# Performance work log

Measured on AMD Instinct MI355X. Metric: run time of the kernel, lower is better.

The kernel has to match this reference:

```python
import jax, jax.numpy as jnp
import numpy as np

B, T, K, H = 4, 2048, 128, 8
MASK = True


def setup_inputs() -> dict:
    key = jax.random.key(0)
    ks = jax.random.split(key, 6)
    s = 0.02
    return {
        "x": jax.random.normal(ks[0], (B, T, K), dtype=jnp.float32),
        "Wq": jax.random.normal(ks[1], (K, H * K), dtype=jnp.float32) * s,
        "Wk": jax.random.normal(ks[2], (K, H * K), dtype=jnp.float32) * s,
        "Wv": jax.random.normal(ks[3], (K, H * K), dtype=jnp.float32) * s,
        "Wu": jax.random.normal(ks[4], (H * K, K), dtype=jnp.float32) * s,
        "bu": jnp.zeros((K,), dtype=jnp.float32),
    }


def reference(x, Wq, Wk, Wv, Wu, bu):
    b, t, k = x.shape
    h = H
    q = (x @ Wq).reshape(b, t, h, k)
    kk = (x @ Wk).reshape(b, t, h, k)
    # module pre-scales values by k**-0.25 (idiosyncratic but faithful)
    v = (x @ Wv).reshape(b, t, h, k) * (k ** -0.25)
    # scores [b, h, t, t], scaled by k**-0.5
    scores = jnp.einsum('bthd,bshd->bhts', q, kk) * (k ** -0.5)
    if MASK:
        causal = jnp.tril(jnp.ones((t, t), dtype=bool))
        scores = jnp.where(causal, scores, -jnp.inf)
    w = jax.nn.softmax(scores, axis=-1)
    out = jnp.einsum('bhts,bshd->bthd', w, v).reshape(b, t, h * k)
    return out @ Wu + bu
```

## Files before the change

### kernel.cpp

```cpp
#include <hip/hip_runtime.h>
#include <hip/hip_bf16.h>
#include <math.h>

#define B_ 4
#define T_ 2048
#define D_ 128
#define H_ 8
#define BT_ 8192
#define HD_ 1024

typedef __attribute__((ext_vector_type(8))) short bf16x8;
typedef __attribute__((ext_vector_type(4))) float f32x4;

__device__ __forceinline__ short f2bf(float f) {
  union { float f; unsigned u; } v; v.f = f;
  return (short)((v.u + 0x8000u) >> 16);
}

#if __has_builtin(__builtin_amdgcn_exp2f)
#define EXP2F(x) __builtin_amdgcn_exp2f(x)
#else
#define EXP2F(x) exp2f(x)
#endif

#define QSCALE 0.12752040242046492f
#define VSCALE 0.29730177875068026f

__device__ __forceinline__ void gld16(const short* g, short* l) {
  __builtin_amdgcn_global_load_lds(
      (const __attribute__((address_space(1))) void*)g,
      (__attribute__((address_space(3))) void*)l, 16, 0, 0);
}

__global__ __launch_bounds__(256) void prep(
    const float* __restrict__ x, const float* __restrict__ Wq,
    const float* __restrict__ Wk, const float* __restrict__ Wv,
    short* __restrict__ xbf, short* __restrict__ WT)
{
  __shared__ __align__(16) short Tt[128*128];
  const int tid = threadIdx.x;
  const int id = blockIdx.x;
  if (id < 24) {
    const int wsel = id >> 3, nt = id & 7;
    const float* W = (wsel == 0) ? Wq : (wsel == 1) ? Wk : Wv;
    #pragma unroll 4
    for (int i = tid; i < 4096; i += 256) {
      int k = i >> 5, n4 = (i & 31) << 2;
      float4 v = *(const float4*)&W[(size_t)k * HD_ + nt*128 + n4];
      float vv[4] = {v.x, v.y, v.z, v.w};
      #pragma unroll
      for (int j = 0; j < 4; j++) {
        int n = n4 + j;
        Tt[n*128 + (((k >> 3) ^ (n & 15)) << 3) + (k & 7)] = f2bf(vv[j]);
      }
    }
    __syncthreads();
    short* dst = WT + (size_t)id * 16384;
    #pragma unroll 2
    for (int i = tid; i < 2048; i += 256)
      *(bf16x8*)&dst[i*8] = *(bf16x8*)&Tt[i*8];
  } else {
    const int xb = id - 24;
    const float* xs = x + (size_t)xb * 16384;
    short* dst = xbf + (size_t)xb * 16384;
    #pragma unroll 4
    for (int i = tid; i < 4096; i += 256) {
      float4 v = ((const float4*)xs)[i];
      int row = i >> 5, c = (i & 31) >> 1, half = i & 1;
      short4 p;
      p.x = f2bf(v.x); p.y = f2bf(v.y); p.z = f2bf(v.z); p.w = f2bf(v.w);
      *(short4*)&dst[(row*16 + (c ^ (row & 15)))*8 + half*4] = p;
    }
  }
}

__global__ __launch_bounds__(256, 2) void qkv_proj(
    const short* __restrict__ xbf, const short* __restrict__ WT,
    short* __restrict__ Qw, short* __restrict__ Kw, short* __restrict__ Vw)
{
  __shared__ __align__(16) short As[16384];
  __shared__ __align__(16) short Bs[16384];
  const int tid = threadIdx.x;
  const int w = tid >> 6, lane = tid & 63, quad = lane >> 4, l16 = lane & 15;
  const int m0 = blockIdx.x * 128;

  {
    const short* asrc = xbf + (size_t)blockIdx.x * 16384;
    const short* bsrc = WT + (size_t)blockIdx.y * 16384;
    const int so = w*4096 + lane*8;
    #pragma unroll
    for (int cc = 0; cc < 8; cc++) {
      gld16(asrc + so + cc*512, &As[w*4096 + cc*512]);
      gld16(bsrc + so + cc*512, &Bs[w*4096 + cc*512]);
    }
  }
  __syncthreads();

  const int wm = (w & 1) * 64, wn = (w >> 1) * 64;
  f32x4 acc[4][4];
  #pragma unroll
  for (int a = 0; a < 4; a++)
    #pragma unroll
    for (int b = 0; b < 4; b++) acc[a][b] = (f32x4){0.f, 0.f, 0.f, 0.f};

  #pragma unroll
  for (int kk = 0; kk < 4; kk++) {
    const int swz = ((kk*4 + quad) ^ l16) << 3;
    bf16x8 af[4], bfv[4];
    #pragma unroll
    for (int mi = 0; mi < 4; mi++) af[mi]  = *(bf16x8*)&As[(wm + mi*16 + l16)*128 + swz];
    #pragma unroll
    for (int ni = 0; ni < 4; ni++) bfv[ni] = *(bf16x8*)&Bs[(wn + ni*16 + l16)*128 + swz];
    #pragma unroll
    for (int mi = 0; mi < 4; mi++)
      #pragma unroll
      for (int ni = 0; ni < 4; ni++)
        acc[mi][ni] = __builtin_amdgcn_mfma_f32_16x16x32_bf16(af[mi], bfv[ni], acc[mi][ni], 0, 0, 0);
  }

  __syncthreads();
  const int wsel = (int)blockIdx.y >> 3;
  #pragma unroll
  for (int mi = 0; mi < 4; mi++) {
    #pragma unroll
    for (int ni = 0; ni < 4; ni++) {
      const int t0l = wm + mi*16 + quad*4;
      const int d   = wn + ni*16 + l16;
      if (wsel == 0) {
        #pragma unroll
        for (int r = 0; r < 4; r++)
          As[(t0l + r)*128 + d] = f2bf(acc[mi][ni][r] * QSCALE);
      } else if (wsel == 1) {
        const int c = d >> 3;
        #pragma unroll
        for (int r = 0; r < 4; r++) {
          const int tl = (t0l + r) & 63, tile = (t0l + r) >> 6;
          As[tile*8192 + tl*128 + ((c ^ (tl & 15)) << 3) + (d & 7)] =
              f2bf(acc[mi][ni][r]);
        }
      } else {
        #pragma unroll
        for (int r = 0; r < 4; r++) {
          const int tl = (t0l + r) & 63, tile = (t0l + r) >> 6;
          As[tile*8192 + d*64 + (((tl >> 3) ^ (d & 7)) << 3) + (tl & 7)] =
              f2bf(acc[mi][ni][r] * VSCALE);
        }
      }
    }
  }
  __syncthreads();

  const int h = (int)blockIdx.y & 7;
  const int b = m0 >> 11, t0 = m0 & 2047;
  short* base = ((wsel == 0) ? Qw : (wsel == 1) ? Kw : Vw)
              + (size_t)(b*H_ + h)*262144 + (size_t)t0*128;
  #pragma unroll 2
  for (int i = tid; i < 2048; i += 256)
    *(bf16x8*)&base[i*8] = *(bf16x8*)&As[i*8];
}

__global__ __launch_bounds__(256, 2) void attn_kernel(
    const short* __restrict__ Qw, const short* __restrict__ Kw,
    const short* __restrict__ Vw, short* __restrict__ attnw)
{
  __shared__ __align__(16) short Ks[2][8192];
  __shared__ __align__(16) short Vs[2][8192];
  __shared__ __align__(16) short Ps[4096];

  const int tid = threadIdx.x;
  const int id = (int)blockIdx.x;
  const int xcd = id & 7;
  const int u   = (id >> 3) & 3;
  const int pid = id >> 5;
  const int bh = xcd | (u << 3);
  const int b = bh >> 3, h = bh & 7;
  const int w = tid >> 6, lane = tid & 63, quad = lane >> 4, l16 = lane & 15;

  const short* Qp = Qw + (size_t)bh * T_ * D_;
  const short* Kp = Kw + (size_t)bh * T_ * D_;
  const short* Vp = Vw + (size_t)bh * D_ * T_;
  short* Pw = &Ps[w*1024];
  const int so = w*2048 + lane*8;

  #pragma unroll 1
  for (int ph = 0; ph < 2; ph++) {
    const int qi = ph ? (31 - pid) : pid;
    const int rowQ = qi*64 + w*16;

    bf16x8 qa[4];
    #pragma unroll
    for (int kk = 0; kk < 4; kk++)
      qa[kk] = *(const bf16x8*)(Qp + (size_t)(rowQ + l16)*D_ + kk*32 + quad*8);

    f32x4 o[8];
    #pragma unroll
    for (int e = 0; e < 8; e++) o[e] = (f32x4){0,0,0,0};
    float l[4] = {0,0,0,0};

    __syncthreads();
    {
      const short* kt = Kp;
      const short* vt = Vp;
      #pragma unroll
      for (int cc = 0; cc < 4; cc++) {
        gld16(kt + so + cc*512, &Ks[0][w*2048 + cc*512]);
        gld16(vt + so + cc*512, &Vs[0][w*2048 + cc*512]);
      }
    }
    int buf = 0;

    for (int it = 0; it <= qi; ++it) {
      __syncthreads();
      if (it < qi) {
        const short* kt = Kp + ((size_t)(it+1) << 13);
        const short* vt = Vp + ((size_t)(it+1) << 13);
        #pragma unroll
        for (int cc = 0; cc < 4; cc++) {
          gld16(kt + so + cc*512, &Ks[buf^1][w*2048 + cc*512]);
          gld16(vt + so + cc*512, &Vs[buf^1][w*2048 + cc*512]);
        }
      }
      const short* ks = &Ks[buf][0];
      const short* vs = &Vs[buf][0];

      f32x4 s[4];
      #pragma unroll
      for (int nj = 0; nj < 4; nj++) s[nj] = (f32x4){0,0,0,0};
      #pragma unroll
      for (int kk = 0; kk < 4; kk++) {
        const int swz = ((kk*4 + quad) ^ l16) << 3;
        #pragma unroll
        for (int nj = 0; nj < 4; nj++) {
          bf16x8 kb = *(const bf16x8*)&ks[(nj*16 + l16)*128 + swz];
          s[nj] = __builtin_amdgcn_mfma_f32_16x16x32_bf16(qa[kk], kb, s[nj], 0, 0, 0);
        }
      }

      if (it < qi) {
        #pragma unroll
        for (int nj = 0; nj < 4; nj++) {
          #pragma unroll
          for (int r = 0; r < 4; r++) {
            float p = EXP2F(s[nj][r]);
            l[r] += p;
            const int row = quad*4 + r, col = nj*16 + l16;
            Pw[row*64 + (((col >> 3) ^ (row & 7)) << 3) + (col & 7)] = f2bf(p);
          }
        }
      } else {
        const int s0 = it * 64;
        #pragma unroll
        for (int nj = 0; nj < 4; nj++) {
          const int key = s0 + nj*16 + l16;
          #pragma unroll
          for (int r = 0; r < 4; r++) {
            float p = (key > rowQ + quad*4 + r) ? 0.f : EXP2F(s[nj][r]);
            l[r] += p;
            const int row = quad*4 + r, col = nj*16 + l16;
            Pw[row*64 + (((col >> 3) ^ (row & 7)) << 3) + (col & 7)] = f2bf(p);
          }
        }
      }

      #pragma unroll
      for (int kk2 = 0; kk2 < 2; kk2++) {
        const int swz = ((kk2*4 + quad) ^ (l16 & 7)) << 3;
        bf16x8 pa = *(bf16x8*)&Pw[l16*64 + swz];
        #pragma unroll
        for (int e = 0; e < 8; e++) {
          bf16x8 vb = *(const bf16x8*)&vs[(e*16 + l16)*64 + swz];
          o[e] = __builtin_amdgcn_mfma_f32_16x16x32_bf16(pa, vb, o[e], 0, 0, 0);
        }
      }
      buf ^= 1;
    }

    #pragma unroll
    for (int r = 0; r < 4; r++) {
      float t = l[r];
      t += __shfl_xor(t, 1); t += __shfl_xor(t, 2);
      t += __shfl_xor(t, 4); t += __shfl_xor(t, 8);
      l[r] = 1.0f / t;
    }
    const size_t tb = ((size_t)((b*2048 + rowQ) >> 5) * 8 + h) * 4096;
    const int row0 = rowQ & 31;
    #pragma unroll
    for (int e = 0; e < 8; e++) {
      const int c = e*2 + (l16 >> 3);
      #pragma unroll
      for (int r = 0; r < 4; r++) {
        const int row = row0 + quad*4 + r;
        attnw[tb + row*128 + ((c ^ (row & 15)) << 3) + (l16 & 7)] =
            f2bf(o[e][r] * l[r]);
      }
    }
  }
}

__global__ __launch_bounds__(256) void wu_prep(
    const float* __restrict__ Wu, short* __restrict__ WuT)
{
  __shared__ __align__(16) short Tt[128*128];
  const int tid = threadIdx.x;
  const int kc = blockIdx.x;
  #pragma unroll 4
  for (int i = tid; i < 4096; i += 256) {
    int kl = i >> 5, n4 = (i & 31) << 2;
    float4 v = *(const float4*)&Wu[(size_t)(kc*128 + kl) * D_ + n4];
    float vv[4] = {v.x, v.y, v.z, v.w};
    #pragma unroll
    for (int j = 0; j < 4; j++) {
      int n = n4 + j;
      Tt[n*128 + (((kl >> 3) ^ (n & 15)) << 3) + (kl & 7)] = f2bf(vv[j]);
    }
  }
  __syncthreads();
  short* dst = WuT + (size_t)kc * 16384;
  #pragma unroll 2
  for (int i = tid; i < 2048; i += 256)
    *(bf16x8*)&dst[i*8] = *(bf16x8*)&Tt[i*8];
}

__global__ __launch_bounds__(256, 2) void out_proj(
    const short* __restrict__ attnw, const short* __restrict__ WuT,
    const float* __restrict__ bu, float* __restrict__ out)
{
  __shared__ __align__(16) short As2[2][2048];
  __shared__ __align__(16) short Bs2[2][16384];
  const int tid = threadIdx.x;
  const int w = tid >> 6, lane = tid & 63, quad = lane >> 4, l16 = lane & 15;
  const int m0 = (int)blockIdx.x * 16;
  const int mtile32 = m0 >> 5, half = (m0 >> 4) & 1;

  f32x4 o2[2];
  o2[0] = (f32x4){0,0,0,0}; o2[1] = (f32x4){0,0,0,0};

  {
    const short* ab = attnw + (size_t)(mtile32*8 + 0)*4096 + half*2048;
    const short* bb = WuT;
    gld16(ab + w*512 + lane*8, &As2[0][w*512]);
    #pragma unroll
    for (int cc = 0; cc < 8; cc++)
      gld16(bb + w*4096 + cc*512 + lane*8, &Bs2[0][w*4096 + cc*512]);
  }
  int buf = 0;

  for (int kc = 0; kc < 8; kc++) {
    __syncthreads();
    if (kc < 7) {
      const short* ab = attnw + (size_t)(mtile32*8 + kc + 1)*4096 + half*2048;
      const short* bb = WuT + (size_t)(kc + 1)*16384;
      gld16(ab + w*512 + lane*8, &As2[buf^1][w*512]);
      #pragma unroll
      for (int cc = 0; cc < 8; cc++)
        gld16(bb + w*4096 + cc*512 + lane*8, &Bs2[buf^1][w*4096 + cc*512]);
    }
    const short* as = &As2[buf][0];
    const short* bs = &Bs2[buf][0];
    #pragma unroll
    for (int kk = 0; kk < 4; kk++) {
      const int swz = ((kk*4 + quad) ^ l16) << 3;
      bf16x8 a = *(const bf16x8*)&as[l16*128 + swz];
      #pragma unroll
      for (int e = 0; e < 2; e++) {
        bf16x8 bfr = *(const bf16x8*)&bs[((w*2 + e)*16 + l16)*128 + swz];
        o2[e] = __builtin_amdgcn_mfma_f32_16x16x32_bf16(a, bfr, o2[e], 0, 0, 0);
      }
    }
    buf ^= 1;
  }

  #pragma unroll
  for (int e = 0; e < 2; e++) {
    const int n = (w*2 + e)*16 + l16;
    const float bias = bu[n];
    #pragma unroll
    for (int r = 0; r < 4; r++) {
      const int m = m0 + quad*4 + r;
      out[(size_t)m*D_ + n] = o2[e][r] + bias;
    }
  }
}

extern "C" void kernel_launch(void* const* d_in, const int* in_sizes, int n_in,
                              void* d_out, int out_size, void* d_ws, size_t ws_size,
                              hipStream_t stream) {
  (void)in_sizes; (void)n_in; (void)out_size; (void)ws_size;
  const float* x  = (const float*)d_in[0];
  const float* Wq = (const float*)d_in[1];
  const float* Wk = (const float*)d_in[2];
  const float* Wv = (const float*)d_in[3];
  const float* Wu = (const float*)d_in[4];
  const float* bu = (const float*)d_in[5];
  float* out = (float*)d_out;

  const size_t headElems = (size_t)B_ * H_ * T_ * D_;
  short* Qw    = (short*)d_ws;
  short* Kw    = Qw + headElems;
  short* Vw    = Kw + headElems;
  short* attnw = Vw + headElems;
  short* xbf = attnw;
  short* WT  = attnw + 1048576;
  short* WuT = Kw;

  prep<<<dim3(88), 256, 0, stream>>>(x, Wq, Wk, Wv, xbf, WT);
  qkv_proj<<<dim3(64, 24), 256, 0, stream>>>(xbf, WT, Qw, Kw, Vw);
  attn_kernel<<<dim3(512), 256, 0, stream>>>(Qw, Kw, Vw, attnw);
  wu_prep<<<dim3(8), 256, 0, stream>>>(Wu, WuT);
  out_proj<<<dim3(512), 256, 0, stream>>>(attnw, WuT, bu, out);
}
```

Baseline: 160.3 us.

## Process paired low/high causal query tiles together sharing each K/V tile load

The attention kernel used to run the low and high query tiles of a causal pair in two sequential phases, loading K/V twice. It now walks the K/V tiles once and computes both query tiles against each shared tile, skipping the low tile once it passes its diagonal. This halves K/V global traffic and removes a phase barrier. Q is now written in the swizzled layout so it matches K, pid is remapped for balance, and output is staged through LDS for coalesced stores. The cost is doubled accumulator registers (two o[8] sets), which risks pressure at two waves per SIMD.

```diff
diff --git a/kernel.cpp b/kernel.cpp
--- a/kernel.cpp
+++ b/kernel.cpp
@@ -126,17 +126,14 @@
     for (int ni = 0; ni < 4; ni++) {
       const int t0l = wm + mi*16 + quad*4;
       const int d   = wn + ni*16 + l16;
-      if (wsel == 0) {
-        #pragma unroll
-        for (int r = 0; r < 4; r++)
-          As[(t0l + r)*128 + d] = f2bf(acc[mi][ni][r] * QSCALE);
-      } else if (wsel == 1) {
+      if (wsel <= 1) {
+        const float sc = wsel ? 1.0f : QSCALE;
         const int c = d >> 3;
         #pragma unroll
         for (int r = 0; r < 4; r++) {
           const int tl = (t0l + r) & 63, tile = (t0l + r) >> 6;
           As[tile*8192 + tl*128 + ((c ^ (tl & 15)) << 3) + (d & 7)] =
-              f2bf(acc[mi][ni][r]);
+              f2bf(acc[mi][ni][r] * sc);
         }
       } else {
         #pragma unroll
@@ -169,99 +166,93 @@
 
   const int tid = threadIdx.x;
   const int id = (int)blockIdx.x;
-  const int xcd = id & 7;
-  const int u   = (id >> 3) & 3;
-  const int pid = id >> 5;
-  const int bh = xcd | (u << 3);
+  const int bh = (id & 7) | (((id >> 3) & 3) << 3);
   const int b = bh >> 3, h = bh & 7;
+  const int m = id >> 5;
+  const int pid = (((m >> 3) ^ (id & 1)) ? 15 - (m & 7) : (m & 7));
+  const int qlo = pid, qhi = 31 - pid;
   const int w = tid >> 6, lane = tid & 63, quad = lane >> 4, l16 = lane & 15;
-
-  const short* Qp = Qw + (size_t)bh * T_ * D_;
-  const short* Kp = Kw + (size_t)bh * T_ * D_;
-  const short* Vp = Vw + (size_t)bh * D_ * T_;
+  const int rowL = qlo*64 + w*16, rowH = qhi*64 + w*16;
+
+  const short* Qp = Qw + (size_t)bh * 262144;
+  const short* Kp = Kw + (size_t)bh * 262144;
+  const short* Vp = Vw + (size_t)bh * 262144;
   short* Pw = &Ps[w*1024];
   const int so = w*2048 + lane*8;
 
-  #pragma unroll 1
-  for (int ph = 0; ph < 2; ph++) {
-    const int qi = ph ? (31 - pid) : pid;
-    const int rowQ = qi*64 + w*16;
-
-    bf16x8 qa[4];
-    #pragma unroll
-    for (int kk = 0; kk < 4; kk++)
-      qa[kk] = *(const bf16x8*)(Qp + (size_t)(rowQ + l16)*D_ + kk*32 + quad*8);
-
-    f32x4 o[8];
-    #pragma unroll
-    for (int e = 0; e < 8; e++) o[e] = (f32x4){0,0,0,0};
-    float l[4] = {0,0,0,0};
-
+  bf16x8 qaL[4], qaH[4];
+  {
+    const int tlL = (rowL & 63) + l16, tiL = rowL >> 6;
+    const int tlH = (rowH & 63) + l16, tiH = rowH >> 6;
+    #pragma unroll
+    for (int kk = 0; kk < 4; kk++) {
+      qaL[kk] = *(const bf16x8*)(Qp + ((size_t)tiL << 13) + tlL*128 +
+                                 (((kk*4 + quad) ^ (tlL & 15)) << 3));
+      qaH[kk] = *(const bf16x8*)(Qp + ((size_t)tiH << 13) + tlH*128 +
+                                 (((kk*4 + quad) ^ (tlH & 15)) << 3));
+    }
+  }
+
+  f32x4 oL[8], oH[8];
+  #pragma unroll
+  for (int e = 0; e < 8; e++) { oL[e] = (f32x4){0,0,0,0}; oH[e] = (f32x4){0,0,0,0}; }
+  float lL[4] = {0,0,0,0}, lH[4] = {0,0,0,0};
+
+  {
+    #pragma unroll
+    for (int cc = 0; cc < 4; cc++) {
+      gld16(Kp + so + cc*512, &Ks[0][w*2048 + cc*512]);
+      gld16(Vp + so + cc*512, &Vs[0][w*2048 + cc*512]);
+    }
+  }
+  int buf = 0;
+  const int nIt = qhi + 1;
+
+  for (int it = 0; it < nIt; ++it) {
     __syncthreads();
+    if (it + 1 < nIt) {
+      const short* kt = Kp + ((size_t)(it+1) << 13);
+      const short* vt = Vp + ((size_t)(it+1) << 13);
+      #pragma unroll
+      for (int cc = 0; cc < 4; cc++) {
+        gld16(kt + so + cc*512, &Ks[buf^1][w*2048 + cc*512]);
+        gld16(vt + so + cc*512, &Vs[buf^1][w*2048 + cc*512]);
+      }
+    }
+    const short* ks = &Ks[buf][0];
+    const short* vs = &Vs[buf][0];
+    const bool doL = (it <= qlo);
+
+    f32x4 sH[4], sL[4];
+    #pragma unroll
+    for (int nj = 0; nj < 4; nj++) { sH[nj] = (f32x4){0,0,0,0}; sL[nj] = (f32x4){0,0,0,0}; }
+    #pragma unroll
+    for (int kk = 0; kk < 4; kk++) {
+      const int swz = ((kk*4 + quad) ^ l16) << 3;
+      #pragma unroll
+      for (int nj = 0; nj < 4; nj++) {
+        bf16x8 kb = *(const bf16x8*)&ks[(nj*16 + l16)*128 + swz];
+        sH[nj] = __builtin_amdgcn_mfma_f32_16x16x32_bf16(qaH[kk], kb, sH[nj], 0, 0, 0);
+        if (doL)
+          sL[nj] = __builtin_amdgcn_mfma_f32_16x16x32_bf16(qaL[kk], kb, sL[nj], 0, 0, 0);
+      }
+    }
+
     {
-      const short* kt = Kp;
-      const short* vt = Vp;
-      #pragma unroll
-      for (int cc = 0; cc < 4; cc++) {
-        gld16(kt + so + cc*512, &Ks[0][w*2048 + cc*512]);
-        gld16(vt + so + cc*512, &Vs[0][w*2048 + cc*512]);
-      }
-    }
-    int buf = 0;
-
-    for (int it = 0; it <= qi; ++it) {
-      __syncthreads();
-      if (it < qi) {
-        const short* kt = Kp + ((size_t)(it+1) << 13);
-        const short* vt = Vp + ((size_t)(it+1) << 13);
-        #pragma unroll
-        for (int cc = 0; cc < 4; cc++) {
-          gld16(kt + so + cc*512, &Ks[buf^1][w*2048 + cc*512]);
-          gld16(vt + so + cc*512, &Vs[buf^1][w*2048 + cc*512]);
-        }
-      }
-      const short* ks = &Ks[buf][0];
-      const short* vs = &Vs[buf][0];
-
-      f32x4 s[4];
-      #pragma unroll
-      for (int nj = 0; nj < 4; nj++) s[nj] = (f32x4){0,0,0,0};
-      #pragma unroll
-      for (int kk = 0; kk < 4; kk++) {
-        const int swz = ((kk*4 + quad) ^ l16) << 3;
-        #pragma unroll
-        for (int nj = 0; nj < 4; nj++) {
-          bf16x8 kb = *(const bf16x8*)&ks[(nj*16 + l16)*128 + swz];
-          s[nj] = __builtin_amdgcn_mfma_f32_16x16x32_bf16(qa[kk], kb, s[nj], 0, 0, 0);
-        }
-      }
-
-      if (it < qi) {
-        #pragma unroll
-        for (int nj = 0; nj < 4; nj++) {
-          #pragma unroll
-          for (int r = 0; r < 4; r++) {
-            float p = EXP2F(s[nj][r]);
-            l[r] += p;
-            const int row = quad*4 + r, col = nj*16 + l16;
-            Pw[row*64 + (((col >> 3) ^ (row & 7)) << 3) + (col & 7)] = f2bf(p);
-          }
-        }
-      } else {
-        const int s0 = it * 64;
-        #pragma unroll
-        for (int nj = 0; nj < 4; nj++) {
-          const int key = s0 + nj*16 + l16;
-          #pragma unroll
-          for (int r = 0; r < 4; r++) {
-            float p = (key > rowQ + quad*4 + r) ? 0.f : EXP2F(s[nj][r]);
-            l[r] += p;
-            const int row = quad*4 + r, col = nj*16 + l16;
-            Pw[row*64 + (((col >> 3) ^ (row & 7)) << 3) + (col & 7)] = f2bf(p);
-          }
-        }
-      }
-
+      const int s0 = it * 64;
+      const bool diag = (it == qhi);
+      #pragma unroll
+      for (int nj = 0; nj < 4; nj++) {
+        const int key = s0 + nj*16 + l16;
+        #pragma unroll
+        for (int r = 0; r < 4; r++) {
+          float p = EXP2F(sH[nj][r]);
+          if (diag) p = (key > rowH + quad*4 + r) ? 0.f : p;
+          lH[r] += p;
+          const int row = quad*4 + r, col = nj*16 + l16;
+          Pw[row*64 + (((col >> 3) ^ (row & 7)) << 3) + (col & 7)] = f2bf(p);
+        }
+      }
       #pragma unroll
       for (int kk2 = 0; kk2 < 2; kk2++) {
         const int swz = ((kk2*4 + quad) ^ (l16 & 7)) << 3;
@@ -269,31 +260,72 @@
         #pragma unroll
         for (int e = 0; e < 8; e++) {
           bf16x8 vb = *(const bf16x8*)&vs[(e*16 + l16)*64 + swz];
-          o[e] = __builtin_amdgcn_mfma_f32_16x16x32_bf16(pa, vb, o[e], 0, 0, 0);
-        }
-      }
-      buf ^= 1;
-    }
-
+          oH[e] = __builtin_amdgcn_mfma_f32_16x16x32_bf16(pa, vb, oH[e], 0, 0, 0);
+        }
+      }
+    }
+    if (doL) {
+      const int s0 = it * 64;
+      const bool diag = (it == qlo);
+      #pragma unroll
+      for (int nj = 0; nj < 4; nj++) {
+        const int key = s0 + nj*16 + l16;
+        #pragma unroll
+        for (int r = 0; r < 4; r++) {
+          float p = EXP2F(sL[nj][r]);
+          if (diag) p = (key > rowL + quad*4 + r) ? 0.f : p;
+          lL[r] += p;
+          const int row = quad*4 + r, col = nj*16 + l16;
+          Pw[row*64 + (((col >> 3) ^ (row & 7)) << 3) + (col & 7)] = f2bf(p);
+        }
+      }
+      #pragma unroll
+      for (int kk2 = 0; kk2 < 2; kk2++) {
+        const int swz = ((kk2*4 + quad) ^ (l16 & 7)) << 3;
+        bf16x8 pa = *(bf16x8*)&Pw[l16*64 + swz];
+        #pragma unroll
+        for (int e = 0; e < 8; e++) {
+          bf16x8 vb = *(const bf16x8*)&vs[(e*16 + l16)*64 + swz];
+          oL[e] = __builtin_amdgcn_mfma_f32_16x16x32_bf16(pa, vb, oL[e], 0, 0, 0);
+        }
+      }
+    }
+    buf ^= 1;
+  }
+
+  #pragma unroll
+  for (int r = 0; r < 4; r++) {
+    float tL = lL[r], tH = lH[r];
+    tL += __shfl_xor(tL, 1); tL += __shfl_xor(tL, 2);
+    tL += __shfl_xor(tL, 4); tL += __shfl_xor(tL, 8);
+    tH += __shfl_xor(tH, 1); tH += __shfl_xor(tH, 2);
+    tH += __shfl_xor(tH, 4); tH += __shfl_xor(tH, 8);
+    lL[r] = 1.0f / tL; lH[r] = 1.0f / tH;
+  }
+  __syncthreads();
+  short* img = &Ks[0][0];
+  #pragma unroll
+  for (int e = 0; e < 8; e++) {
+    const int c = e*2 + (l16 >> 3);
     #pragma unroll
     for (int r = 0; r < 4; r++) {
-      float t = l[r];
-      t += __shfl_xor(t, 1); t += __shfl_xor(t, 2);
-      t += __shfl_xor(t, 4); t += __shfl_xor(t, 8);
-      l[r] = 1.0f / t;
-    }
-    const size_t tb = ((size_t)((b*2048 + rowQ) >> 5) * 8 + h) * 4096;
-    const int row0 = rowQ & 31;
-    #pragma unroll
-    for (int e = 0; e < 8; e++) {
-      const int c = e*2 + (l16 >> 3);
-      #pragma unroll
-      for (int r = 0; r < 4; r++) {
-        const int row = row0 + quad*4 + r;
-        attnw[tb + row*128 + ((c ^ (row & 15)) << 3) + (l16 & 7)] =
-            f2bf(o[e][r] * l[r]);
-      }
-    }
+      const int lrow = w*16 + quad*4 + r;
+      const int sub = lrow >> 5, r32 = lrow & 31;
+      const int off = sub*4096 + r32*128 + ((c ^ (r32 & 15)) << 3) + (l16 & 7);
+      img[off]        = f2bf(oL[e][r] * lL[r]);
+      img[8192 + off] = f2bf(oH[e][r] * lH[r]);
+    }
+  }
+  __syncthreads();
+  const int stL = b*64 + qlo*2, stH = b*64 + qhi*2;
+  #pragma unroll
+  for (int seg = 0; seg < 4; seg++) {
+    const int st = ((seg < 2) ? stL : stH) + (seg & 1);
+    short* dst = attnw + ((size_t)st*8 + h)*4096;
+    const short* src = img + seg*4096;
+    #pragma unroll
+    for (int i = tid; i < 512; i += 256)
+      *(bf16x8*)&dst[i*8] = *(const bf16x8*)&src[i*8];
   }
 }
 
@@ -336,12 +368,11 @@
   o2[0] = (f32x4){0,0,0,0}; o2[1] = (f32x4){0,0,0,0};
 
   {
-    const short* ab = attnw + (size_t)(mtile32*8 + 0)*4096 + half*2048;
-    const short* bb = WuT;
+    const short* ab = attnw + (size_t)(mtile32*8)*4096 + half*2048;
     gld16(ab + w*512 + lane*8, &As2[0][w*512]);
     #pragma unroll
     for (int cc = 0; cc < 8; cc++)
-      gld16(bb + w*4096 + cc*512 + lane*8, &Bs2[0][w*4096 + cc*512]);
+      gld16(WuT + w*4096 + cc*512 + lane*8, &Bs2[0][w*4096 + cc*512]);
   }
   int buf = 0;
 
@@ -376,8 +407,8 @@
     const float bias = bu[n];
     #pragma unroll
     for (int r = 0; r < 4; r++) {
-      const int m = m0 + quad*4 + r;
-      out[(size_t)m*D_ + n] = o2[e][r] + bias;
+      const int mm = m0 + quad*4 + r;
+      out[(size_t)mm*D_ + n] = o2[e][r] + bias;
     }
   }
 }
```

Result: slower. 182.8 us (+14.1%).

## Split attention into one block per query tile and single-buffer K/V

Applied to the files above, without the earlier changes.

The attention kernel now launches one block per 64-row query tile instead of pairing two tiles per block. The query-to-block mapping is balanced across XCDs, K/V staging is single-buffered, and the occupancy hint rises from 2 to 4 blocks per SM. The aim is more concurrent blocks to hide latency, at the cost of losing the prefetch overlap between K/V tiles. The output is staged through LDS for coalesced stores. The QKV projection swaps operand roles for Q/K so it can write packed short4 stores into swizzled layouts, and Q is now read in that swizzled layout.

```diff
diff --git a/kernel.cpp b/kernel.cpp
--- a/kernel.cpp
+++ b/kernel.cpp
@@ -96,7 +96,11 @@
   }
   __syncthreads();
 
-  const int wm = (w & 1) * 64, wn = (w >> 1) * 64;
+  const int wsel = (int)blockIdx.y >> 3;
+  const int rA0 = (w & 1) * 64, rB0 = (w >> 1) * 64;
+  const short* RA = (wsel <= 1) ? Bs : As;
+  const short* RB = (wsel <= 1) ? As : Bs;
+
   f32x4 acc[4][4];
   #pragma unroll
   for (int a = 0; a < 4; a++)
@@ -108,43 +112,48 @@
     const int swz = ((kk*4 + quad) ^ l16) << 3;
     bf16x8 af[4], bfv[4];
     #pragma unroll
-    for (int mi = 0; mi < 4; mi++) af[mi]  = *(bf16x8*)&As[(wm + mi*16 + l16)*128 + swz];
-    #pragma unroll
-    for (int ni = 0; ni < 4; ni++) bfv[ni] = *(bf16x8*)&Bs[(wn + ni*16 + l16)*128 + swz];
-    #pragma unroll
-    for (int mi = 0; mi < 4; mi++)
-      #pragma unroll
-      for (int ni = 0; ni < 4; ni++)
-        acc[mi][ni] = __builtin_amdgcn_mfma_f32_16x16x32_bf16(af[mi], bfv[ni], acc[mi][ni], 0, 0, 0);
-  }
-
-  __syncthreads();
-  const int wsel = (int)blockIdx.y >> 3;
-  #pragma unroll
-  for (int mi = 0; mi < 4; mi++) {
-    #pragma unroll
-    for (int ni = 0; ni < 4; ni++) {
-      const int t0l = wm + mi*16 + quad*4;
-      const int d   = wn + ni*16 + l16;
-      if (wsel == 0) {
-        #pragma unroll
-        for (int r = 0; r < 4; r++)
-          As[(t0l + r)*128 + d] = f2bf(acc[mi][ni][r] * QSCALE);
-      } else if (wsel == 1) {
-        const int c = d >> 3;
-        #pragma unroll
-        for (int r = 0; r < 4; r++) {
-          const int tl = (t0l + r) & 63, tile = (t0l + r) >> 6;
-          As[tile*8192 + tl*128 + ((c ^ (tl & 15)) << 3) + (d & 7)] =
-              f2bf(acc[mi][ni][r]);
-        }
-      } else {
-        #pragma unroll
-        for (int r = 0; r < 4; r++) {
-          const int tl = (t0l + r) & 63, tile = (t0l + r) >> 6;
-          As[tile*8192 + d*64 + (((tl >> 3) ^ (d & 7)) << 3) + (tl & 7)] =
-              f2bf(acc[mi][ni][r] * VSCALE);
-        }
+    for (int ai = 0; ai < 4; ai++) af[ai]  = *(const bf16x8*)&RA[(rA0 + ai*16 + l16)*128 + swz];
+    #pragma unroll
+    for (int bi = 0; bi < 4; bi++) bfv[bi] = *(const bf16x8*)&RB[(rB0 + bi*16 + l16)*128 + swz];
+    #pragma unroll
+    for (int ai = 0; ai < 4; ai++)
+      #pragma unroll
+      for (int bi = 0; bi < 4; bi++)
+        acc[ai][bi] = __builtin_amdgcn_mfma_f32_16x16x32_bf16(af[ai], bfv[bi], acc[ai][bi], 0, 0, 0);
+  }
+
+  __syncthreads();
+  if (wsel <= 1) {
+    const float sc = wsel ? 1.0f : QSCALE;
+    #pragma unroll
+    for (int ai = 0; ai < 4; ai++) {
+      #pragma unroll
+      for (int bi = 0; bi < 4; bi++) {
+        const int d0 = rA0 + ai*16 + quad*4;
+        const int t  = rB0 + bi*16 + l16;
+        const int tile = t >> 6, tl = t & 63;
+        short4 p;
+        p.x = f2bf(acc[ai][bi][0] * sc);
+        p.y = f2bf(acc[ai][bi][1] * sc);
+        p.z = f2bf(acc[ai][bi][2] * sc);
+        p.w = f2bf(acc[ai][bi][3] * sc);
+        *(short4*)&As[tile*8192 + tl*128 + (((d0 >> 3) ^ (tl & 15)) << 3) + (d0 & 7)] = p;
+      }
+    }
+  } else {
+    #pragma unroll
+    for (int ai = 0; ai < 4; ai++) {
+      #pragma unroll
+      for (int bi = 0; bi < 4; bi++) {
+        const int t0 = rA0 + ai*16 + quad*4;
+        const int d  = rB0 + bi*16 + l16;
+        const int tile = t0 >> 6, tl0 = t0 & 63;
+        short4 p;
+        p.x = f2bf(acc[ai][bi][0] * VSCALE);
+        p.y = f2bf(acc[ai][bi][1] * VSCALE);
+        p.z = f2bf(acc[ai][bi][2] * VSCALE);
+        p.w = f2bf(acc[ai][bi][3] * VSCALE);
+        *(short4*)&As[tile*8192 + d*64 + (((tl0 >> 3) ^ (d & 7)) << 3) + (tl0 & 7)] = p;
       }
     }
   }
@@ -159,141 +168,141 @@
     *(bf16x8*)&base[i*8] = *(bf16x8*)&As[i*8];
 }
 
-__global__ __launch_bounds__(256, 2) void attn_kernel(
+__global__ __launch_bounds__(256, 4) void attn_kernel(
     const short* __restrict__ Qw, const short* __restrict__ Kw,
     const short* __restrict__ Vw, short* __restrict__ attnw)
 {
-  __shared__ __align__(16) short Ks[2][8192];
-  __shared__ __align__(16) short Vs[2][8192];
+  __shared__ __align__(16) short Ks[8192];
+  __shared__ __align__(16) short Vs[8192];
   __shared__ __align__(16) short Ps[4096];
 
   const int tid = threadIdx.x;
   const int id = (int)blockIdx.x;
   const int xcd = id & 7;
-  const int u   = (id >> 3) & 3;
-  const int pid = id >> 5;
+  const int j   = id >> 3;
+  const int u   = j & 3;
+  const int q   = (j >> 2) & 7;
+  const int vv  = (j >> 5) & 3;
+  const int slot = u ^ vv;
+  const int qi = (slot == 0) ? q : (slot == 1) ? 15 - q
+               : (slot == 2) ? 16 + q : 31 - q;
   const int bh = xcd | (u << 3);
   const int b = bh >> 3, h = bh & 7;
   const int w = tid >> 6, lane = tid & 63, quad = lane >> 4, l16 = lane & 15;
-
-  const short* Qp = Qw + (size_t)bh * T_ * D_;
-  const short* Kp = Kw + (size_t)bh * T_ * D_;
-  const short* Vp = Vw + (size_t)bh * D_ * T_;
+  const int rowQ = qi*64 + w*16;
+
+  const short* Qp = Qw + (size_t)bh * 262144;
+  const short* Kp = Kw + (size_t)bh * 262144;
+  const short* Vp = Vw + (size_t)bh * 262144;
+
+  bf16x8 qa[4];
+  {
+    const int tl = (rowQ & 63) + l16;
+    const short* qp = Qp + ((size_t)(rowQ >> 6) << 13) + tl*128;
+    #pragma unroll
+    for (int kk = 0; kk < 4; kk++)
+      qa[kk] = *(const bf16x8*)(qp + (((kk*4 + quad) ^ (tl & 15)) << 3));
+  }
+
+  f32x4 o[8];
+  #pragma unroll
+  for (int e = 0; e < 8; e++) o[e] = (f32x4){0,0,0,0};
+  float l[4] = {0,0,0,0};
+
   short* Pw = &Ps[w*1024];
   const int so = w*2048 + lane*8;
-
-  #pragma unroll 1
-  for (int ph = 0; ph < 2; ph++) {
-    const int qi = ph ? (31 - pid) : pid;
-    const int rowQ = qi*64 + w*16;
-
-    bf16x8 qa[4];
-    #pragma unroll
-    for (int kk = 0; kk < 4; kk++)
-      qa[kk] = *(const bf16x8*)(Qp + (size_t)(rowQ + l16)*D_ + kk*32 + quad*8);
-
-    f32x4 o[8];
-    #pragma unroll
-    for (int e = 0; e < 8; e++) o[e] = (f32x4){0,0,0,0};
-    float l[4] = {0,0,0,0};
-
+  const int nIter = qi + 1;
+
+  for (int it = 0; it < nIter; ++it) {
+    if (it) __syncthreads();
+    {
+      const short* kt = Kp + ((size_t)it << 13);
+      const short* vt = Vp + ((size_t)it << 13);
+      #pragma unroll
+      for (int cc = 0; cc < 4; cc++) {
+        gld16(kt + so + cc*512, &Ks[w*2048 + cc*512]);
+        gld16(vt + so + cc*512, &Vs[w*2048 + cc*512]);
+      }
+    }
     __syncthreads();
-    {
-      const short* kt = Kp;
-      const short* vt = Vp;
-      #pragma unroll
-      for (int cc = 0; cc < 4; cc++) {
-        gld16(kt + so + cc*512, &Ks[0][w*2048 + cc*512]);
-        gld16(vt + so + cc*512, &Vs[0][w*2048 + cc*512]);
-      }
-    }
-    int buf = 0;
-
-    for (int it = 0; it <= qi; ++it) {
-      __syncthreads();
-      if (it < qi) {
-        const short* kt = Kp + ((size_t)(it+1) << 13);
-        const short* vt = Vp + ((size_t)(it+1) << 13);
+
+    f32x4 s[4];
+    #pragma unroll
+    for (int nj = 0; nj < 4; nj++) s[nj] = (f32x4){0,0,0,0};
+    #pragma unroll
+    for (int kk = 0; kk < 4; kk++) {
+      const int swz = ((kk*4 + quad) ^ l16) << 3;
+      #pragma unroll
+      for (int nj = 0; nj < 4; nj++) {
+        bf16x8 kb = *(const bf16x8*)&Ks[(nj*16 + l16)*128 + swz];
+        s[nj] = __builtin_amdgcn_mfma_f32_16x16x32_bf16(qa[kk], kb, s[nj], 0, 0, 0);
+      }
+    }
+
+    if (it < qi) {
+      #pragma unroll
+      for (int nj = 0; nj < 4; nj++) {
         #pragma unroll
-        for (int cc = 0; cc < 4; cc++) {
-          gld16(kt + so + cc*512, &Ks[buf^1][w*2048 + cc*512]);
-          gld16(vt + so + cc*512, &Vs[buf^1][w*2048 + cc*512]);
+        for (int r = 0; r < 4; r++) {
+          float p = EXP2F(s[nj][r]);
+          l[r] += p;
+          const int row = quad*4 + r, col = nj*16 + l16;
+          Pw[row*64 + (((col >> 3) ^ (row & 7)) << 3) + (col & 7)] = f2bf(p);
         }
       }
-      const short* ks = &Ks[buf][0];
-      const short* vs = &Vs[buf][0];
-
-      f32x4 s[4];
-      #pragma unroll
-      for (int nj = 0; nj < 4; nj++) s[nj] = (f32x4){0,0,0,0};
-      #pragma unroll
-      for (int kk = 0; kk < 4; kk++) {
-        const int swz = ((kk*4 + quad) ^ l16) << 3;
+    } else {
+      const int s0 = it * 64;
+      #pragma unroll
+      for (int nj = 0; nj < 4; nj++) {
+        const int key = s0 + nj*16 + l16;
         #pragma unroll
-        for (int nj = 0; nj < 4; nj++) {
-          bf16x8 kb = *(const bf16x8*)&ks[(nj*16 + l16)*128 + swz];
-          s[nj] = __builtin_amdgcn_mfma_f32_16x16x32_bf16(qa[kk], kb, s[nj], 0, 0, 0);
+        for (int r = 0; r < 4; r++) {
+          float p = (key > rowQ + quad*4 + r) ? 0.f : EXP2F(s[nj][r]);
+          l[r] += p;
+          const int row = quad*4 + r, col = nj*16 + l16;
+          Pw[row*64 + (((col >> 3) ^ (row & 7)) << 3) + (col & 7)] = f2bf(p);
         }
       }
-
-      if (it < qi) {
-        #pragma unroll
-        for (int nj = 0; nj < 4; nj++) {
-          #pragma unroll
-          for (int r = 0; r < 4; r++) {
-            float p = EXP2F(s[nj][r]);
-            l[r] += p;
-            const int row = quad*4 + r, col = nj*16 + l16;
-            Pw[row*64 + (((col >> 3) ^ (row & 7)) << 3) + (col & 7)] = f2bf(p);
-          }
-        }
-      } else {
-        const int s0 = it * 64;
-        #pragma unroll
-        for (int nj = 0; nj < 4; nj++) {
-          const int key = s0 + nj*16 + l16;
-          #pragma unroll
-          for (int r = 0; r < 4; r++) {
-            float p = (key > rowQ + quad*4 + r) ? 0.f : EXP2F(s[nj][r]);
-            l[r] += p;
-            const int row = quad*4 + r, col = nj*16 + l16;
-            Pw[row*64 + (((col >> 3) ^ (row & 7)) << 3) + (col & 7)] = f2bf(p);
-          }
-        }
-      }
-
-      #pragma unroll
-      for (int kk2 = 0; kk2 < 2; kk2++) {
-        const int swz = ((kk2*4 + quad) ^ (l16 & 7)) << 3;
-        bf16x8 pa = *(bf16x8*)&Pw[l16*64 + swz];
-        #pragma unroll
-        for (int e = 0; e < 8; e++) {
-          bf16x8 vb = *(const bf16x8*)&vs[(e*16 + l16)*64 + swz];
-          o[e] = __builtin_amdgcn_mfma_f32_16x16x32_bf16(pa, vb, o[e], 0, 0, 0);
-        }
-      }
-      buf ^= 1;
-    }
-
+    }
+
+    #pragma unroll
+    for (int kk2 = 0; kk2 < 2; kk2++) {
+      const int swz = ((kk2*4 + quad) ^ (l16 & 7)) << 3;
+      bf16x8 pa = *(bf16x8*)&Pw[l16*64 + swz];
+      #pragma unroll
+      for (int e = 0; e < 8; e++) {
+        bf16x8 vb = *(const bf16x8*)&Vs[(e*16 + l16)*64 + swz];
+        o[e] = __builtin_amdgcn_mfma_f32_16x16x32_bf16(pa, vb, o[e], 0, 0, 0);
+      }
+    }
+  }
+
+  #pragma unroll
+  for (int r = 0; r < 4; r++) {
+    float t = l[r];
+    t += __shfl_xor(t, 1); t += __shfl_xor(t, 2);
+    t += __shfl_xor(t, 4); t += __shfl_xor(t, 8);
+    l[r] = 1.0f / t;
+  }
+  __syncthreads();
+  #pragma unroll
+  for (int e = 0; e < 8; e++) {
+    const int c = e*2 + (l16 >> 3);
     #pragma unroll
     for (int r = 0; r < 4; r++) {
-      float t = l[r];
-      t += __shfl_xor(t, 1); t += __shfl_xor(t, 2);
-      t += __shfl_xor(t, 4); t += __shfl_xor(t, 8);
-      l[r] = 1.0f / t;
-    }
-    const size_t tb = ((size_t)((b*2048 + rowQ) >> 5) * 8 + h) * 4096;
-    const int row0 = rowQ & 31;
-    #pragma unroll
-    for (int e = 0; e < 8; e++) {
-      const int c = e*2 + (l16 >> 3);
-      #pragma unroll
-      for (int r = 0; r < 4; r++) {
-        const int row = row0 + quad*4 + r;
-        attnw[tb + row*128 + ((c ^ (row & 15)) << 3) + (l16 & 7)] =
-            f2bf(o[e][r] * l[r]);
-      }
-    }
+      const int lrow = w*16 + quad*4 + r;
+      const int sub = lrow >> 5, r32 = lrow & 31;
+      Ks[sub*4096 + r32*128 + ((c ^ (r32 & 15)) << 3) + (l16 & 7)] =
+          f2bf(o[e][r] * l[r]);
+    }
+  }
+  __syncthreads();
+  const int st0 = b*64 + qi*2;
+  #pragma unroll 2
+  for (int i = tid; i < 1024; i += 256) {
+    const int sub = i >> 9, rem = i & 511;
+    short* dst = attnw + ((size_t)(st0 + sub)*8 + h)*4096 + rem*8;
+    *(bf16x8*)dst = *(const bf16x8*)&Ks[i*8];
   }
 }
 
@@ -336,12 +345,11 @@
   o2[0] = (f32x4){0,0,0,0}; o2[1] = (f32x4){0,0,0,0};
 
   {
-    const short* ab = attnw + (size_t)(mtile32*8 + 0)*4096 + half*2048;
-    const short* bb = WuT;
+    const short* ab = attnw + (size_t)(mtile32*8)*4096 + half*2048;
     gld16(ab + w*512 + lane*8, &As2[0][w*512]);
     #pragma unroll
     for (int cc = 0; cc < 8; cc++)
-      gld16(bb + w*4096 + cc*512 + lane*8, &Bs2[0][w*4096 + cc*512]);
+      gld16(WuT + w*4096 + cc*512 + lane*8, &Bs2[0][w*4096 + cc*512]);
   }
   int buf = 0;
 
@@ -376,8 +384,8 @@
     const float bias = bu[n];
     #pragma unroll
     for (int r = 0; r < 4; r++) {
-      const int m = m0 + quad*4 + r;
-      out[(size_t)m*D_ + n] = o2[e][r] + bias;
+      const int mm = m0 + quad*4 + r;
+      out[(size_t)mm*D_ + n] = o2[e][r] + bias;
     }
   }
 }
@@ -405,7 +413,7 @@
 
   prep<<<dim3(88), 256, 0, stream>>>(x, Wq, Wk, Wv, xbf, WT);
   qkv_proj<<<dim3(64, 24), 256, 0, stream>>>(xbf, WT, Qw, Kw, Vw);
-  attn_kernel<<<dim3(512), 256, 0, stream>>>(Qw, Kw, Vw, attnw);
+  attn_kernel<<<dim3(1024), 256, 0, stream>>>(Qw, Kw, Vw, attnw);
   wu_prep<<<dim3(8), 256, 0, stream>>>(Wu, WuT);
   out_proj<<<dim3(512), 256, 0, stream>>>(attnw, WuT, bu, out);
 }
```

Result: no change. 159.2 us (-0.6%).
